# Performance work log

Measured on AMD Instinct MI355X. Metric: run time of the kernel, lower is better.

Reference implementation:

```python
import jax, jax.numpy as jnp
import numpy as np

NUM_HEADS = 16
EPS = 1e-6
NEG_INF = -1e9


def layer_norm(x, scale, bias):
    m = jnp.mean(x, axis=-1, keepdims=True)
    v = jnp.mean(jnp.square(x - m), axis=-1, keepdims=True)
    return (x - m) * jax.lax.rsqrt(v + EPS) * scale + bias


def mha(x_q, x_kv, wq, wk, wv, wo, causal):
    B, Sq, D = x_q.shape
    Sk = x_kv.shape[1]
    H = NUM_HEADS
    Dh = D // H
    q = (x_q @ wq).reshape(B, Sq, H, Dh) * (1.0 / np.sqrt(Dh))
    k = (x_kv @ wk).reshape(B, Sk, H, Dh)
    v = (x_kv @ wv).reshape(B, Sk, H, Dh)
    scores = jnp.einsum('bqhf,bkhf->bhqk', q, k)  # [B,H,Sq,Sk]
    if causal:
        mask = jnp.tril(jnp.ones((Sq, Sk), dtype=bool))
        scores = jnp.where(mask, scores, NEG_INF)
    p = jax.nn.softmax(scores, axis=-1)
    o = jnp.einsum('bhqk,bkhf->bqhf', p, v).reshape(B, Sq, D)
    return o @ wo


def setup_inputs() -> dict:
    key = jax.random.key(0)
    ks = jax.random.split(key, 12)
    B, S, D, F = 2, 2048, 1024, 4096
    w = 0.02
    return {
        'targets': jax.random.normal(ks[0], (B, S, D), jnp.float32),
        'encoded': jax.random.normal(ks[1], (B, S, D), jnp.float32),
        'ln1_s': jnp.ones((D,), jnp.float32),
        'ln1_b': jnp.zeros((D,), jnp.float32),
        'sa_wq': jax.random.normal(ks[2], (D, D), jnp.float32) * w,
        'sa_wk': jax.random.normal(ks[3], (D, D), jnp.float32) * w,
        'sa_wv': jax.random.normal(ks[4], (D, D), jnp.float32) * w,
        'sa_wo': jax.random.normal(ks[5], (D, D), jnp.float32) * w,
        'ln2_s': jnp.ones((D,), jnp.float32),
        'ln2_b': jnp.zeros((D,), jnp.float32),
        'ca_wq': jax.random.normal(ks[6], (D, D), jnp.float32) * w,
        'ca_wk': jax.random.normal(ks[7], (D, D), jnp.float32) * w,
        'ca_wv': jax.random.normal(ks[8], (D, D), jnp.float32) * w,
        'ca_wo': jax.random.normal(ks[9], (D, D), jnp.float32) * w,
        'ln3_s': jnp.ones((D,), jnp.float32),
        'ln3_b': jnp.zeros((D,), jnp.float32),
        'mlp_w1': jax.random.normal(ks[10], (D, F), jnp.float32) * w,
        'mlp_b1': jnp.zeros((F,), jnp.float32),
        'mlp_w2': jax.random.normal(ks[11], (F, D), jnp.float32) * w,
        'mlp_b2': jnp.zeros((D,), jnp.float32),
    }


def reference(targets, encoded, ln1_s, ln1_b, sa_wq, sa_wk, sa_wv, sa_wo,
              ln2_s, ln2_b, ca_wq, ca_wk, ca_wv, ca_wo,
              ln3_s, ln3_b, mlp_w1, mlp_b1, mlp_w2, mlp_b2):
    # Pre-LN causal self-attention + residual
    x = layer_norm(targets, ln1_s, ln1_b)
    x = mha(x, x, sa_wq, sa_wk, sa_wv, sa_wo, causal=True)
    x = x + targets
    # Pre-LN cross-attention over encoder output + residual
    y = layer_norm(x, ln2_s, ln2_b)
    y = mha(y, encoded, ca_wq, ca_wk, ca_wv, ca_wo, causal=False)
    y = y + x
    # Pre-LN MLP + residual
    z = layer_norm(y, ln3_s, ln3_b)
    z = jax.nn.relu(z @ mlp_w1 + mlp_b1) @ mlp_w2 + mlp_b2
    return y + z
```

## Files before the change

kernel.cpp:

```cpp
#include <hip/hip_runtime.h>


#define DEV __device__ __forceinline__

typedef __attribute__((ext_vector_type(8))) _Float16 half8;
typedef __attribute__((ext_vector_type(4))) _Float16 half4;
typedef __attribute__((ext_vector_type(2))) _Float16 half2v;
typedef __attribute__((ext_vector_type(4))) float    f32x4;

#define GLB(p) ((const __attribute__((address_space(1))) void*)(p))
#define LDS(p) ((__attribute__((address_space(3))) void*)(p))

DEV half2v pk(float a, float b) {
  return __builtin_bit_cast(half2v, __builtin_amdgcn_cvt_pkrtz(a, b));
}
DEV half4 pk4(float a, float b, float c, float d) {
  half2v lo = pk(a, b), hi = pk(c, d);
  half4 r; r.x = lo.x; r.y = lo.y; r.z = hi.x; r.w = hi.y;
  return r;
}

DEV float wave_sum_f(float v) {
  #pragma unroll
  for (int off = 32; off; off >>= 1) v += __shfl_xor(v, off);
  return v;
}

struct WtArgs { const float* w[8]; _Float16* wt[8]; };

__global__ __launch_bounds__(256) void wt_square(WtArgs a) {
  const float* w = a.w[blockIdx.z];
  _Float16* wt = a.wt[blockIdx.z];
  __shared__ float t[32][33];
  const int tx = threadIdx.x, ty = threadIdx.y;
  const int n0 = blockIdx.x * 32, k0 = blockIdx.y * 32;
  #pragma unroll
  for (int i = ty; i < 32; i += 8)
    t[i][tx] = w[(size_t)(k0 + i) * 1024 + n0 + tx];
  __syncthreads();
  #pragma unroll
  for (int i = ty; i < 32; i += 8)
    wt[(size_t)(n0 + i) * 1024 + k0 + tx] = (_Float16)t[tx][i];
}

__global__ __launch_bounds__(256) void wt_one(const float* __restrict__ w,
                                              _Float16* __restrict__ wt,
                                              int K, int N) {
  __shared__ float t[32][33];
  const int tx = threadIdx.x, ty = threadIdx.y;
  const int n0 = blockIdx.x * 32, k0 = blockIdx.y * 32;
  #pragma unroll
  for (int i = ty; i < 32; i += 8)
    t[i][tx] = w[(size_t)(k0 + i) * N + n0 + tx];
  __syncthreads();
  #pragma unroll
  for (int i = ty; i < 32; i += 8)
    wt[(size_t)(n0 + i) * K + k0 + tx] = (_Float16)t[tx][i];
}

__global__ __launch_bounds__(256) void cvt_f16(const float* __restrict__ in,
                                               _Float16* __restrict__ out) {
  const size_t i = ((size_t)blockIdx.x * 256 + threadIdx.x) * 4;
  const float4 v = *(const float4*)(in + i);
  *(half4*)(out + i) = pk4(v.x, v.y, v.z, v.w);
}

__global__ __launch_bounds__(256) void ln_kernel(const float* __restrict__ x,
                                                 const float* __restrict__ sc,
                                                 const float* __restrict__ bi,
                                                 _Float16* __restrict__ out) {
  const int row = blockIdx.x;
  const int t = threadIdx.x;
  const float4 v = ((const float4*)(x + (size_t)row * 1024))[t];
  float s  = v.x + v.y + v.z + v.w;
  float s2 = v.x * v.x + v.y * v.y + v.z * v.z + v.w * v.w;
  s = wave_sum_f(s); s2 = wave_sum_f(s2);
  __shared__ float red[8];
  const int lane = t & 63, wid = t >> 6;
  if (lane == 0) { red[wid] = s; red[4 + wid] = s2; }
  __syncthreads();
  s  = red[0] + red[1] + red[2] + red[3];
  s2 = red[4] + red[5] + red[6] + red[7];
  const float mean = s * (1.f / 1024.f);
  const float rstd = rsqrtf(s2 * (1.f / 1024.f) - mean * mean + 1e-6f);
  const float4 sv = ((const float4*)sc)[t];
  const float4 bv = ((const float4*)bi)[t];
  half4 o = pk4((v.x - mean) * rstd * sv.x + bv.x,
                (v.y - mean) * rstd * sv.y + bv.y,
                (v.z - mean) * rstd * sv.z + bv.z,
                (v.w - mean) * rstd * sv.w + bv.w);
  ((half4*)(out + (size_t)row * 1024))[t] = o;
}

template <int EPI, int BM, int BN, int BK>
__global__ __launch_bounds__(256)
void gemm_f16(const _Float16* __restrict__ A, const _Float16* __restrict__ Bt,
              void* __restrict__ Cout, const float* __restrict__ bias,
              const float* __restrict__ resid, int M, int N, int K,
              float scl, int sclCols, _Float16* __restrict__ vt, int vcol0) {
  constexpr int AM = BM / 32;
  constexpr int AN = BN / 32;
  constexpr int RA = BM * BK / 2048;
  constexpr int RB = BN * BK / 2048;
  constexpr int TPR = BK / 8;
  constexpr int RPR = 2048 / BK;
  __shared__ _Float16 As[2][BM * BK];
  __shared__ _Float16 Bs[2][BN * BK];
  const int tid = threadIdx.x;
  const int lane = tid & 63, wid = tid >> 6;
  const int wm = wid >> 1, wn = wid & 1;
  const int q = lane >> 4, m15 = lane & 15;
  const int bm = blockIdx.y, bn = blockIdx.x;

  const int trow = tid / TPR;
  const int tcol = (tid % TPR) * 8;
  const _Float16* Ab = A + ((size_t)bm * BM + trow) * K + tcol;
  const _Float16* Bb = Bt + ((size_t)bn * BN + trow) * K + tcol;

  f32x4 acc[AM][AN] = {};

  auto stage = [&](int k0, int buf) {
    #pragma unroll
    for (int r = 0; r < RA; r++)
      __builtin_amdgcn_global_load_lds(GLB(Ab + (size_t)r * RPR * K + k0),
                                       LDS(&As[buf][r * 2048 + wid * 512]), 16, 0, 0);
    #pragma unroll
    for (int r = 0; r < RB; r++)
      __builtin_amdgcn_global_load_lds(GLB(Bb + (size_t)r * RPR * K + k0),
                                       LDS(&Bs[buf][r * 2048 + wid * 512]), 16, 0, 0);
  };

  stage(0, 0);
  const int nit = K / BK;
  for (int it = 0; it < nit; it++) {
    const int buf = it & 1;
    __syncthreads();
    if (it + 1 < nit) stage((it + 1) * BK, buf ^ 1);
    #pragma unroll
    for (int kk = 0; kk < BK / 32; kk++) {
      half8 af[AM], bf[AN];
      #pragma unroll
      for (int i = 0; i < AM; i++)
        af[i] = *(const half8*)&As[buf][(wm * (BM / 2) + i * 16 + m15) * BK + kk * 32 + q * 8];
      #pragma unroll
      for (int i = 0; i < AN; i++)
        bf[i] = *(const half8*)&Bs[buf][(wn * (BN / 2) + i * 16 + m15) * BK + kk * 32 + q * 8];
      #pragma unroll
      for (int mi = 0; mi < AM; mi++)
        #pragma unroll
        for (int ni = 0; ni < AN; ni++)
          acc[mi][ni] = __builtin_amdgcn_mfma_f32_16x16x32_f16(af[mi], bf[ni],
                                                               acc[mi][ni], 0, 0, 0);
    }
  }

  const int rowbase = bm * BM + wm * (BM / 2);
  const int colbase = bn * BN + wn * (BN / 2);
  #pragma unroll
  for (int ni = 0; ni < AN; ni++) {
    const int col = colbase + ni * 16 + m15;
    float bv = 0.f;
    if (EPI == 2 || EPI == 4) bv = bias[col];
    const float cs = (EPI == 1 || EPI == 5) ? (col < sclCols ? scl : 1.f) : 1.f;
    if (EPI == 5 && col >= vcol0) {
      const int d = col & 63, hh = (col >> 6) & 15;
      #pragma unroll
      for (int mi = 0; mi < AM; mi++) {
        const int row = rowbase + mi * 16 + q * 4;
        const int bb = row >> 11, ss = row & 2047;
        half4 ov = pk4(acc[mi][ni][0], acc[mi][ni][1],
                       acc[mi][ni][2], acc[mi][ni][3]);
        *(half4*)(vt + ((size_t)(bb * 16 + hh) * 64 + d) * 2048 + ss) = ov;
      }
      continue;
    }
    #pragma unroll
    for (int mi = 0; mi < AM; mi++) {
      #pragma unroll
      for (int r = 0; r < 4; r++) {
        const int row = rowbase + mi * 16 + q * 4 + r;
        const size_t idx = (size_t)row * N + col;
        float v = acc[mi][ni][r];
        if (EPI == 1 || EPI == 5) {
          ((_Float16*)Cout)[idx] = (_Float16)(v * cs);
        } else if (EPI == 2) {
          v += bv; v = v > 0.f ? v : 0.f;
          ((_Float16*)Cout)[idx] = (_Float16)v;
        } else if (EPI == 3) {
          ((float*)Cout)[idx] = v + resid[idx];
        } else {
          ((float*)Cout)[idx] = v + bv + resid[idx];
        }
      }
    }
  }
}

__global__ __launch_bounds__(128)
void flash_attn(const _Float16* __restrict__ Q, int qs,
                const _Float16* __restrict__ Kp, int ks,
                const _Float16* __restrict__ Vt, _Float16* __restrict__ O,
                int S, int Sk, int causal) {
  __shared__ _Float16 Ks[64 * 72];
  __shared__ _Float16 Vs[64 * 72];
  __shared__ _Float16 Pq[2][32 * 72];
  const int tid = threadIdx.x;
  const int lane = tid & 63, wid = tid >> 6;
  const int quad = lane >> 4, c15 = lane & 15;
  const int h = blockIdx.y, b = blockIdx.z;
  int qb = blockIdx.x;
  if (causal) qb = (qb & 1) ? ((int)gridDim.x - 1 - (qb >> 1)) : (qb >> 1);
  const int qw0 = qb * 64 + wid * 32;

  half8 qf[2][2];
  #pragma unroll
  for (int nt = 0; nt < 2; nt++)
    #pragma unroll
    for (int kk = 0; kk < 2; kk++)
      qf[nt][kk] = *(const half8*)(Q + (size_t)(b * S + qw0 + nt * 16 + c15) * qs +
                                   h * 64 + kk * 32 + quad * 8);

  f32x4 oacc[4][2];
  #pragma unroll
  for (int i = 0; i < 4; i++)
    #pragma unroll
    for (int j = 0; j < 2; j++)
      oacc[i][j] = (f32x4){0.f, 0.f, 0.f, 0.f};
  float lpart[2] = {0.f, 0.f};

  const int ntiles = causal ? (qb + 1) : (Sk >> 6);
  const _Float16* Kg = Kp + (size_t)b * Sk * ks + h * 64;
  const _Float16* Vg = Vt + (size_t)(b * 16 + h) * 64 * Sk;

  const int srow = tid >> 3, sg8 = (tid & 7) * 8;
  half8 rk[4], rv[4];
  auto ldkv = [&](int jb) {
    #pragma unroll
    for (int i = 0; i < 4; i++) {
      rk[i] = *(const half8*)(Kg + (size_t)(jb + srow + i * 16) * ks + sg8);
      rv[i] = *(const half8*)(Vg + (size_t)(srow + i * 16) * Sk + jb + sg8);
    }
  };
  ldkv(0);

  for (int t = 0; t < ntiles; t++) {
    const int jb = t * 64;
    __syncthreads();
    #pragma unroll
    for (int i = 0; i < 4; i++) {
      *(half8*)&Ks[(srow + i * 16) * 72 + sg8] = rk[i];
      *(half8*)&Vs[(srow + i * 16) * 72 + sg8] = rv[i];
    }
    __syncthreads();
    if (t + 1 < ntiles) ldkv(jb + 64);

    f32x4 s[4][2];
    #pragma unroll
    for (int mt = 0; mt < 4; mt++) {
      const half8 kf0 = *(const half8*)&Ks[(mt * 16 + c15) * 72 + quad * 8];
      const half8 kf1 = *(const half8*)&Ks[(mt * 16 + c15) * 72 + 32 + quad * 8];
      #pragma unroll
      for (int nt = 0; nt < 2; nt++) {
        f32x4 z = {0.f, 0.f, 0.f, 0.f};
        z = __builtin_amdgcn_mfma_f32_16x16x32_f16(kf0, qf[nt][0], z, 0, 0, 0);
        z = __builtin_amdgcn_mfma_f32_16x16x32_f16(kf1, qf[nt][1], z, 0, 0, 0);
        s[mt][nt] = z;
      }
    }

    if (causal && jb + 63 > qw0) {
      #pragma unroll
      for (int mt = 0; mt < 4; mt++)
        #pragma unroll
        for (int nt = 0; nt < 2; nt++) {
          const int qglob = qw0 + nt * 16 + c15;
          #pragma unroll
          for (int rr = 0; rr < 4; rr++) {
            const int kglob = jb + mt * 16 + quad * 4 + rr;
            if (kglob > qglob) s[mt][nt][rr] = -1e30f;
          }
        }
    }

    #pragma unroll
    for (int nt = 0; nt < 2; nt++) {
      float psum = 0.f;
      #pragma unroll
      for (int mt = 0; mt < 4; mt++) {
        #pragma unroll
        for (int rr = 0; rr < 4; rr++) {
          const float p = exp2f(s[mt][nt][rr]);
          s[mt][nt][rr] = p;
          psum += p;
        }
      }
      lpart[nt] += psum;
      #pragma unroll
      for (int mtk = 0; mtk < 4; mtk++) {
        *(half4*)&Pq[wid][(nt * 16 + c15) * 72 + mtk * 16 + quad * 4] =
            pk4(s[mtk][nt][0], s[mtk][nt][1], s[mtk][nt][2], s[mtk][nt][3]);
      }
    }

    half8 pb[2][2];
    #pragma unroll
    for (int kk = 0; kk < 2; kk++)
      #pragma unroll
      for (int nt = 0; nt < 2; nt++)
        pb[kk][nt] = *(const half8*)&Pq[wid][(nt * 16 + c15) * 72 + kk * 32 + quad * 8];
    #pragma unroll
    for (int mtd = 0; mtd < 4; mtd++) {
      const half8 vf0 = *(const half8*)&Vs[(mtd * 16 + c15) * 72 + quad * 8];
      const half8 vf1 = *(const half8*)&Vs[(mtd * 16 + c15) * 72 + 32 + quad * 8];
      #pragma unroll
      for (int nt = 0; nt < 2; nt++) {
        oacc[mtd][nt] = __builtin_amdgcn_mfma_f32_16x16x32_f16(vf0, pb[0][nt],
                                                               oacc[mtd][nt], 0, 0, 0);
        oacc[mtd][nt] = __builtin_amdgcn_mfma_f32_16x16x32_f16(vf1, pb[1][nt],
                                                               oacc[mtd][nt], 0, 0, 0);
      }
    }
  }

  #pragma unroll
  for (int nt = 0; nt < 2; nt++) {
    float l = lpart[nt];
    l += __shfl_xor(l, 16);
    l += __shfl_xor(l, 32);
    const float linv = 1.f / l;
    #pragma unroll
    for (int mtd = 0; mtd < 4; mtd++) {
      half4 ov = pk4(oacc[mtd][nt][0] * linv, oacc[mtd][nt][1] * linv,
                     oacc[mtd][nt][2] * linv, oacc[mtd][nt][3] * linv);
      *(half4*)(O + (size_t)(b * S + qw0 + nt * 16 + c15) * 1024 +
                h * 64 + mtd * 16 + quad * 4) = ov;
    }
  }
}

extern "C" void kernel_launch(void* const* d_in, const int* in_sizes, int n_in,
                              void* d_out, int out_size, void* d_ws, size_t ws_size,
                              hipStream_t stream) {
  const float* targets = (const float*)d_in[0];
  const float* encoded = (const float*)d_in[1];
  const float* ln1_s = (const float*)d_in[2];
  const float* ln1_b = (const float*)d_in[3];
  const float* sa_wq = (const float*)d_in[4];
  const float* sa_wk = (const float*)d_in[5];
  const float* sa_wv = (const float*)d_in[6];
  const float* sa_wo = (const float*)d_in[7];
  const float* ln2_s = (const float*)d_in[8];
  const float* ln2_b = (const float*)d_in[9];
  const float* ca_wq = (const float*)d_in[10];
  const float* ca_wk = (const float*)d_in[11];
  const float* ca_wv = (const float*)d_in[12];
  const float* ca_wo = (const float*)d_in[13];
  const float* ln3_s = (const float*)d_in[14];
  const float* ln3_b = (const float*)d_in[15];
  const float* mlp_w1 = (const float*)d_in[16];
  const float* mlp_b1 = (const float*)d_in[17];
  const float* mlp_w2 = (const float*)d_in[18];
  const float* mlp_b2 = (const float*)d_in[19];

  const int B = 2, S = 2048, D = 1024, F = 4096, M = B * S;
  const size_t MB = 1024ull * 1024ull;
  const float QSCALE = 0.125f * 1.44269504f;
  char* ws = (char*)d_ws;
  _Float16* wsq   = (_Float16*)(ws);
  _Float16* w1t   = (_Float16*)(ws + 16 * MB);
  _Float16* w2t   = (_Float16*)(ws + 24 * MB);
  _Float16* Abf   = (_Float16*)(ws + 32 * MB);
  _Float16* encbf = (_Float16*)(ws + 40 * MB);
  _Float16* QKV   = (_Float16*)(ws + 48 * MB);
  _Float16* Qcb   = (_Float16*)(ws + 48 * MB);
  _Float16* KVb   = (_Float16*)(ws + 56 * MB);
  _Float16* h1    = (_Float16*)(ws + 48 * MB);
  _Float16* Vtb   = (_Float16*)(ws + 80 * MB);
  _Float16* Aob   = (_Float16*)(ws + 88 * MB);
  float*    xres  = (float*)(ws + 96 * MB);
  float*    yres  = (float*)(ws + 112 * MB);

  {
    WtArgs wa;
    const float* sw[8] = {sa_wq, sa_wk, sa_wv, sa_wo, ca_wq, ca_wk, ca_wv, ca_wo};
    for (int i = 0; i < 8; i++) { wa.w[i] = sw[i]; wa.wt[i] = wsq + (size_t)i * D * D; }
    wt_square<<<dim3(32, 32, 8), dim3(32, 8), 0, stream>>>(wa);
  }
  wt_one<<<dim3(F / 32, D / 32), dim3(32, 8), 0, stream>>>(mlp_w1, w1t, D, F);
  wt_one<<<dim3(D / 32, F / 32), dim3(32, 8), 0, stream>>>(mlp_w2, w2t, F, D);
  cvt_f16<<<(M * D) / 1024, 256, 0, stream>>>(encoded, encbf);

  const dim3 gA(S / 64, 16, B);

  ln_kernel<<<M, 256, 0, stream>>>(targets, ln1_s, ln1_b, Abf);
  gemm_f16<5, 128, 128, 32><<<dim3(3072 / 128, M / 128), 256, 0, stream>>>(
      Abf, wsq, QKV, nullptr, nullptr, M, 3072, D, QSCALE, 1024, Vtb, 2048);
  flash_attn<<<gA, 128, 0, stream>>>(QKV, 3072, QKV + 1024, 3072, Vtb, Aob, S, S, 1);
  gemm_f16<3, 64, 64, 64><<<dim3(1024 / 64, M / 64), 256, 0, stream>>>(
      Aob, wsq + 3ull * D * D, xres, nullptr, targets, M, D, D, 1.f, 0, nullptr, 0);

  ln_kernel<<<M, 256, 0, stream>>>(xres, ln2_s, ln2_b, Abf);
  gemm_f16<1, 64, 64, 64><<<dim3(1024 / 64, M / 64), 256, 0, stream>>>(
      Abf, wsq + 4ull * D * D, Qcb, nullptr, nullptr, M, D, D, QSCALE, 1024, nullptr, 0);
  gemm_f16<5, 64, 128, 32><<<dim3(2048 / 128, M / 64), 256, 0, stream>>>(
      encbf, wsq + 5ull * D * D, KVb, nullptr, nullptr, M, 2048, D, 1.f, 0, Vtb, 1024);
  flash_attn<<<gA, 128, 0, stream>>>(Qcb, 1024, KVb, 2048, Vtb, Aob, S, S, 0);
  gemm_f16<3, 64, 64, 64><<<dim3(1024 / 64, M / 64), 256, 0, stream>>>(
      Aob, wsq + 7ull * D * D, yres, nullptr, xres, M, D, D, 1.f, 0, nullptr, 0);

  ln_kernel<<<M, 256, 0, stream>>>(yres, ln3_s, ln3_b, Abf);
  gemm_f16<2, 128, 128, 32><<<dim3(F / 128, M / 128), 256, 0, stream>>>(
      Abf, w1t, h1, mlp_b1, nullptr, M, F, D, 1.f, 0, nullptr, 0);
  gemm_f16<4, 64, 64, 64><<<dim3(1024 / 64, M / 64), 256, 0, stream>>>(
      h1, w2t, (float*)d_out, mlp_b2, yres, M, D, F, 1.f, 0, nullptr, 0);

  (void)in_sizes; (void)n_in; (void)out_size; (void)ws_size;
}
```

Baseline: 590.3 us.

## Split flash attention over KV halves, load K/V directly, retile N=1024 GEMMs

Flash attention now splits each query block's KV range into two halves run by separate blocks. Each block writes unnormalized fp16 partial outputs and row sums, and a new attn_combine kernel adds the two halves and normalizes. The goal is twice as many blocks, and shorter, more even causal work per block. The block index is remapped so each XCD handles a contiguous set of batch-heads, which should improve L2 reuse. The LDS staging of K/V with its syncthreads is removed in favour of direct per-lane global loads, and launch bounds raise occupancy. The N=1024 GEMMs move from 64x64 to 128x64 tiles. Costs: an extra kernel and a partial-output round trip through memory, duplicate K/V global reads across the two waves, and fp16 rounding of unnormalized partials.

New measurement: 673.9 us. +14.2%, slower.

```diff
diff --git a/kernel.cpp b/kernel.cpp
--- a/kernel.cpp
+++ b/kernel.cpp
@@ -196,20 +196,27 @@
   }
 }
 
-__global__ __launch_bounds__(128)
+__global__ __launch_bounds__(128, 4)
 void flash_attn(const _Float16* __restrict__ Q, int qs,
                 const _Float16* __restrict__ Kp, int ks,
-                const _Float16* __restrict__ Vt, _Float16* __restrict__ O,
+                const _Float16* __restrict__ Vt,
+                _Float16* __restrict__ Opart, float* __restrict__ Lpart,
                 int S, int Sk, int causal) {
-  __shared__ _Float16 Ks[64 * 72];
-  __shared__ _Float16 Vs[64 * 72];
   __shared__ _Float16 Pq[2][32 * 72];
   const int tid = threadIdx.x;
   const int lane = tid & 63, wid = tid >> 6;
   const int quad = lane >> 4, c15 = lane & 15;
-  const int h = blockIdx.y, b = blockIdx.z;
-  int qb = blockIdx.x;
-  if (causal) qb = (qb & 1) ? ((int)gridDim.x - 1 - (qb >> 1)) : (qb >> 1);
+
+  const int gx = gridDim.x;
+  const int lid = blockIdx.x + gx * (blockIdx.y + 16 * blockIdx.z);
+  const int xcd = lid & 7, slot = lid >> 3;
+  const int bh = xcd * 4 + (slot / gx);
+  const int qs2 = slot % gx;
+  const int h = bh & 15, b = bh >> 4;
+  int qb = qs2 >> 1;
+  const int split = qs2 & 1;
+  const int NQB = gx >> 1;
+  if (causal) qb = (qb & 1) ? (NQB - 1 - (qb >> 1)) : (qb >> 1);
   const int qw0 = qb * 64 + wid * 32;
 
   half8 qf[2][2];
@@ -228,37 +235,24 @@
       oacc[i][j] = (f32x4){0.f, 0.f, 0.f, 0.f};
   float lpart[2] = {0.f, 0.f};
 
-  const int ntiles = causal ? (qb + 1) : (Sk >> 6);
-  const _Float16* Kg = Kp + (size_t)b * Sk * ks + h * 64;
-  const _Float16* Vg = Vt + (size_t)(b * 16 + h) * 64 * Sk;
-
-  const int srow = tid >> 3, sg8 = (tid & 7) * 8;
-  half8 rk[4], rv[4];
-  auto ldkv = [&](int jb) {
-    #pragma unroll
-    for (int i = 0; i < 4; i++) {
-      rk[i] = *(const half8*)(Kg + (size_t)(jb + srow + i * 16) * ks + sg8);
-      rv[i] = *(const half8*)(Vg + (size_t)(srow + i * 16) * Sk + jb + sg8);
-    }
-  };
-  ldkv(0);
-
-  for (int t = 0; t < ntiles; t++) {
-    const int jb = t * 64;
-    __syncthreads();
-    #pragma unroll
-    for (int i = 0; i < 4; i++) {
-      *(half8*)&Ks[(srow + i * 16) * 72 + sg8] = rk[i];
-      *(half8*)&Vs[(srow + i * 16) * 72 + sg8] = rv[i];
-    }
-    __syncthreads();
-    if (t + 1 < ntiles) ldkv(jb + 64);
+  const int ntF = causal ? (qb + 1) : (Sk >> 6);
+  const int nA = (ntF + 1) >> 1;
+  const int t0 = split ? nA : 0;
+  const int t1 = split ? ntF : nA;
+
+  const _Float16* Kl = Kp + (size_t)b * Sk * ks + h * 64 +
+                       (size_t)c15 * ks + quad * 8;
+  const _Float16* Vl = Vt + (size_t)(b * 16 + h) * 64 * Sk +
+                       (size_t)c15 * Sk + quad * 8;
+
+  for (int t = t0; t < t1; t++) {
+    const int jb = t << 6;
 
     f32x4 s[4][2];
     #pragma unroll
     for (int mt = 0; mt < 4; mt++) {
-      const half8 kf0 = *(const half8*)&Ks[(mt * 16 + c15) * 72 + quad * 8];
-      const half8 kf1 = *(const half8*)&Ks[(mt * 16 + c15) * 72 + 32 + quad * 8];
+      const half8 kf0 = *(const half8*)(Kl + (size_t)(jb + mt * 16) * ks);
+      const half8 kf1 = *(const half8*)(Kl + (size_t)(jb + mt * 16) * ks + 32);
       #pragma unroll
       for (int nt = 0; nt < 2; nt++) {
         f32x4 z = {0.f, 0.f, 0.f, 0.f};
@@ -310,8 +304,8 @@
         pb[kk][nt] = *(const half8*)&Pq[wid][(nt * 16 + c15) * 72 + kk * 32 + quad * 8];
     #pragma unroll
     for (int mtd = 0; mtd < 4; mtd++) {
-      const half8 vf0 = *(const half8*)&Vs[(mtd * 16 + c15) * 72 + quad * 8];
-      const half8 vf1 = *(const half8*)&Vs[(mtd * 16 + c15) * 72 + 32 + quad * 8];
+      const half8 vf0 = *(const half8*)(Vl + (size_t)(mtd * 16) * Sk + jb);
+      const half8 vf1 = *(const half8*)(Vl + (size_t)(mtd * 16) * Sk + jb + 32);
       #pragma unroll
       for (int nt = 0; nt < 2; nt++) {
         oacc[mtd][nt] = __builtin_amdgcn_mfma_f32_16x16x32_f16(vf0, pb[0][nt],
@@ -322,20 +316,41 @@
     }
   }
 
+  _Float16* Ob = Opart + (size_t)split * ((size_t)2 * S * 1024) +
+                 (size_t)b * S * 1024;
   #pragma unroll
   for (int nt = 0; nt < 2; nt++) {
     float l = lpart[nt];
     l += __shfl_xor(l, 16);
     l += __shfl_xor(l, 32);
-    const float linv = 1.f / l;
+    const int qrow = qw0 + nt * 16 + c15;
+    if (quad == 0)
+      Lpart[((size_t)(split * 2 + b) * 16 + h) * S + qrow] = l;
     #pragma unroll
     for (int mtd = 0; mtd < 4; mtd++) {
-      half4 ov = pk4(oacc[mtd][nt][0] * linv, oacc[mtd][nt][1] * linv,
-                     oacc[mtd][nt][2] * linv, oacc[mtd][nt][3] * linv);
-      *(half4*)(O + (size_t)(b * S + qw0 + nt * 16 + c15) * 1024 +
-                h * 64 + mtd * 16 + quad * 4) = ov;
+      half4 ov = pk4(oacc[mtd][nt][0], oacc[mtd][nt][1],
+                     oacc[mtd][nt][2], oacc[mtd][nt][3]);
+      *(half4*)(Ob + (size_t)qrow * 1024 + h * 64 + mtd * 16 + quad * 4) = ov;
     }
   }
+}
+
+__global__ __launch_bounds__(256)
+void attn_combine(const _Float16* __restrict__ Op, const float* __restrict__ Lp,
+                  _Float16* __restrict__ O) {
+  const int row = blockIdx.x, tid = threadIdx.x;
+  const int col = tid << 2, h = tid >> 4;
+  const int b = row >> 11, sq = row & 2047;
+  const float la = Lp[((size_t)(b * 16 + h)) * 2048 + sq];
+  const float lb = Lp[((size_t)((b + 2) * 16 + h)) * 2048 + sq];
+  const float linv = 1.f / (la + lb);
+  const half4 pa = *(const half4*)(Op + (size_t)row * 1024 + col);
+  const half4 pb = *(const half4*)(Op + ((size_t)4096 + row) * 1024 + col);
+  half4 o = pk4(((float)pa.x + (float)pb.x) * linv,
+                ((float)pa.y + (float)pb.y) * linv,
+                ((float)pa.z + (float)pb.z) * linv,
+                ((float)pa.w + (float)pb.w) * linv);
+  *(half4*)(O + (size_t)row * 1024 + col) = o;
 }
 
 extern "C" void kernel_launch(void* const* d_in, const int* in_sizes, int n_in,
@@ -375,10 +390,12 @@
   _Float16* Qcb   = (_Float16*)(ws + 48 * MB);
   _Float16* KVb   = (_Float16*)(ws + 56 * MB);
   _Float16* h1    = (_Float16*)(ws + 48 * MB);
+  float*    Lbuf  = (float*)(ws + 72 * MB);
   _Float16* Vtb   = (_Float16*)(ws + 80 * MB);
   _Float16* Aob   = (_Float16*)(ws + 88 * MB);
   float*    xres  = (float*)(ws + 96 * MB);
   float*    yres  = (float*)(ws + 112 * MB);
+  _Float16* Opart = (_Float16*)(ws + 112 * MB);
 
   {
     WtArgs wa;
@@ -390,28 +407,32 @@
   wt_one<<<dim3(D / 32, F / 32), dim3(32, 8), 0, stream>>>(mlp_w2, w2t, F, D);
   cvt_f16<<<(M * D) / 1024, 256, 0, stream>>>(encoded, encbf);
 
-  const dim3 gA(S / 64, 16, B);
+  const dim3 gA(2 * (S / 64), 16, B);
 
   ln_kernel<<<M, 256, 0, stream>>>(targets, ln1_s, ln1_b, Abf);
   gemm_f16<5, 128, 128, 32><<<dim3(3072 / 128, M / 128), 256, 0, stream>>>(
       Abf, wsq, QKV, nullptr, nullptr, M, 3072, D, QSCALE, 1024, Vtb, 2048);
-  flash_attn<<<gA, 128, 0, stream>>>(QKV, 3072, QKV + 1024, 3072, Vtb, Aob, S, S, 1);
-  gemm_f16<3, 64, 64, 64><<<dim3(1024 / 64, M / 64), 256, 0, stream>>>(
+  flash_attn<<<gA, 128, 0, stream>>>(QKV, 3072, QKV + 1024, 3072, Vtb,
+                                     Opart, Lbuf, S, S, 1);
+  attn_combine<<<M, 256, 0, stream>>>(Opart, Lbuf, Aob);
+  gemm_f16<3, 128, 64, 64><<<dim3(1024 / 64, M / 128), 256, 0, stream>>>(
       Aob, wsq + 3ull * D * D, xres, nullptr, targets, M, D, D, 1.f, 0, nullptr, 0);
 
   ln_kernel<<<M, 256, 0, stream>>>(xres, ln2_s, ln2_b, Abf);
-  gemm_f16<1, 64, 64, 64><<<dim3(1024 / 64, M / 64), 256, 0, stream>>>(
+  gemm_f16<1, 128, 64, 64><<<dim3(1024 / 64, M / 128), 256, 0, stream>>>(
       Abf, wsq + 4ull * D * D, Qcb, nullptr, nullptr, M, D, D, QSCALE, 1024, nullptr, 0);
   gemm_f16<5, 64, 128, 32><<<dim3(2048 / 128, M / 64), 256, 0, stream>>>(
       encbf, wsq + 5ull * D * D, KVb, nullptr, nullptr, M, 2048, D, 1.f, 0, Vtb, 1024);
-  flash_attn<<<gA, 128, 0, stream>>>(Qcb, 1024, KVb, 2048, Vtb, Aob, S, S, 0);
-  gemm_f16<3, 64, 64, 64><<<dim3(1024 / 64, M / 64), 256, 0, stream>>>(
+  flash_attn<<<gA, 128, 0, stream>>>(Qcb, 1024, KVb, 2048, Vtb,
+                                     Opart, Lbuf, S, S, 0);
+  attn_combine<<<M, 256, 0, stream>>>(Opart, Lbuf, Aob);
+  gemm_f16<3, 128, 64, 64><<<dim3(1024 / 64, M / 128), 256, 0, stream>>>(
       Aob, wsq + 7ull * D * D, yres, nullptr, xres, M, D, D, 1.f, 0, nullptr, 0);
 
   ln_kernel<<<M, 256, 0, stream>>>(yres, ln3_s, ln3_b, Abf);
   gemm_f16<2, 128, 128, 32><<<dim3(F / 128, M / 128), 256, 0, stream>>>(
       Abf, w1t, h1, mlp_b1, nullptr, M, F, D, 1.f, 0, nullptr, 0);
-  gemm_f16<4, 64, 64, 64><<<dim3(1024 / 64, M / 64), 256, 0, stream>>>(
+  gemm_f16<4, 128, 64, 64><<<dim3(1024 / 64, M / 128), 256, 0, stream>>>(
       h1, w2t, (float*)d_out, mlp_b2, yres, M, D, F, 1.f, 0, nullptr, 0);
 
   (void)in_sizes; (void)n_in; (void)out_size; (void)ws_size;
```
